# Kernel tuning notes

Measured on AMD Instinct MI355X. Metric: run time of the kernel, lower is better.

The kernel has to match this reference:

```python
import jax, jax.numpy as jnp
import numpy as np
import math

HEADS = 8
CH = 16  # hidden_channels per head
SCALE = 1.0 / math.sqrt(CH)


def _transformer_conv(x, src, dst, qw, qb, kw, kb, vw, vb, sw, sb):
    """PyG TransformerConv (concat=True, root_weight=True, eval mode -> no dropout)."""
    N = x.shape[0]
    q = (x @ qw + qb).reshape(N, HEADS, CH)
    k = (x @ kw + kb).reshape(N, HEADS, CH)
    v = (x @ vw + vb).reshape(N, HEADS, CH)
    # per-edge attention logits: message from src j to dst i
    alpha = jnp.sum(q[dst] * k[src], axis=-1) * SCALE        # [E, H]
    # segment softmax over incoming edges of each dst node
    m = jax.ops.segment_max(alpha, dst, num_segments=N)      # [N, H]
    a = jnp.exp(alpha - m[dst])                              # [E, H]
    denom = jax.ops.segment_sum(a, dst, num_segments=N)      # [N, H]
    a = a / denom[dst]
    msg = v[src] * a[:, :, None]                             # [E, H, C]
    out = jax.ops.segment_sum(msg, dst, num_segments=N).reshape(N, HEADS * CH)
    return out + x @ sw + sb  # skip connection (lin_skip)


def setup_inputs() -> dict:
    key = jax.random.key(0)
    ks = jax.random.split(key, 16)
    N, E, IN = 50000, 800000, 128
    D = HEADS * CH  # 128

    def lin(k, fi, fo):
        return (jax.random.normal(k, (fi, fo), jnp.float32) / math.sqrt(fi))

    inp = {
        "x": jax.random.normal(ks[0], (N, IN), jnp.float32),
        "edge_index": jax.random.randint(ks[1], (2, E), 0, N, dtype=jnp.int64),
        "edge_attr": jax.random.normal(ks[2], (E, 1), jnp.float32),
        # conv1: in_channels -> hidden*heads
        "q_w0": lin(ks[3], IN, D), "q_b0": jnp.zeros((D,), jnp.float32),
        "k_w0": lin(ks[4], IN, D), "k_b0": jnp.zeros((D,), jnp.float32),
        "v_w0": lin(ks[5], IN, D), "v_b0": jnp.zeros((D,), jnp.float32),
        "s_w0": lin(ks[6], IN, D), "s_b0": jnp.zeros((D,), jnp.float32),
        # conv2[0]: hidden*heads -> hidden*heads
        "q_w1": lin(ks[7], D, D), "q_b1": jnp.zeros((D,), jnp.float32),
        "k_w1": lin(ks[8], D, D), "k_b1": jnp.zeros((D,), jnp.float32),
        "v_w1": lin(ks[9], D, D), "v_b1": jnp.zeros((D,), jnp.float32),
        "s_w1": lin(ks[10], D, D), "s_b1": jnp.zeros((D,), jnp.float32),
    }
    return inp


def reference(x, edge_index, edge_attr,
              q_w0, q_b0, k_w0, k_b0, v_w0, v_b0, s_w0, s_b0,
              q_w1, q_b1, k_w1, k_b1, v_w1, v_b1, s_w1, s_b1):
    src, dst = edge_index[0], edge_index[1]
    # edge_attr is accepted but unused by the original forward
    h = _transformer_conv(x, src, dst, q_w0, q_b0, k_w0, k_b0, v_w0, v_b0, s_w0, s_b0)
    h = jax.nn.relu(h)
    h = _transformer_conv(h, src, dst, q_w1, q_b1, k_w1, k_b1, v_w1, v_b1, s_w1, s_b1)
    return h
```

## Files before the change

### kernel.cpp

```cpp
#include <hip/hip_runtime.h>
#include <math.h>


#define HEADS 8
#define CH 16
#define DM 128
#define SCALE 0.25f

typedef __attribute__((ext_vector_type(8))) short short8;
typedef __attribute__((ext_vector_type(4))) float floatx4;
typedef __attribute__((ext_vector_type(2))) float floatx2;

static __device__ __forceinline__ ushort f2bf(float f) {
    unsigned u = __float_as_uint(f);
    unsigned r = u + 0x7FFFu + ((u >> 16) & 1u);
    return (ushort)(r >> 16);
}
static __device__ __forceinline__ float bflo(unsigned u) {
    return __uint_as_float(u << 16);
}
static __device__ __forceinline__ float bfhi(unsigned u) {
    return __uint_as_float(u & 0xFFFF0000u);
}
static __device__ __forceinline__ unsigned pack2bf(float lo, float hi) {
    return (unsigned)f2bf(lo) | ((unsigned)f2bf(hi) << 16);
}
static __device__ __forceinline__ floatx2 fp8lo(unsigned v) {
    return __builtin_amdgcn_cvt_pk_f32_fp8(v, false);
}
static __device__ __forceinline__ floatx2 fp8hi(unsigned v) {
    return __builtin_amdgcn_cvt_pk_f32_fp8(v, true);
}

#define AP 136

static __device__ __forceinline__ void gemm_body(
    int bx, const float* __restrict__ Xf, const ushort* __restrict__ Xb,
    const ushort* __restrict__ WT,
    const float* __restrict__ bq, const float* __restrict__ bk,
    const float* __restrict__ bv, const float* __restrict__ bsk,
    ushort* __restrict__ Qb, ushort* __restrict__ Kb,
    unsigned char* __restrict__ Vq, ushort* __restrict__ Sb, int N,
    ushort* As)
{
    const int row0 = bx * 32;
    const int tid  = threadIdx.x;

    if (Xf) {
        #pragma unroll
        for (int i = 0; i < 2; ++i) {
            int id = tid + i * 512;
            int r = id >> 5, ch = id & 31;
            float4 v = make_float4(0.f, 0.f, 0.f, 0.f);
            if (row0 + r < N)
                v = *(const float4*)(Xf + (size_t)(row0 + r) * DM + ch * 4);
            ushort4 sv;
            sv.x = f2bf(v.x); sv.y = f2bf(v.y);
            sv.z = f2bf(v.z); sv.w = f2bf(v.w);
            *(ushort4*)(As + r * AP + ch * 4) = sv;
        }
    } else {
        int id = tid;
        int r = id >> 4, ch = id & 15;
        uint4 v = make_uint4(0, 0, 0, 0);
        if (row0 + r < N)
            v = *(const uint4*)(Xb + (size_t)(row0 + r) * DM + ch * 8);
        *(uint4*)(As + r * AP + ch * 8) = v;
    }
    __syncthreads();

    const int lane = tid & 63, w = tid >> 6;
    const int band = w & 3;
    const int m0   = (w >> 2) * 2;
    const int lr = lane & 15, lq = lane >> 4;

    short8 a[4][2];
    #pragma unroll
    for (int ks = 0; ks < 4; ++ks) {
        const int koff = ks * 32 + lq * 8;
        #pragma unroll
        for (int mt = 0; mt < 2; ++mt)
            a[ks][mt] = *(const short8*)(As + (mt * 16 + lr) * AP + koff);
    }

    #pragma unroll
    for (int mi = 0; mi < 2; ++mi) {
        const int mat = m0 + mi;
        const ushort* Wband = WT + (size_t)mat * 16384 + (size_t)band * 4096;
        const float* bias = (mat == 0) ? bq : (mat == 1) ? bk
                          : (mat == 2) ? bv : bsk;
        floatx4 acc[2][2] = {};
        #pragma unroll
        for (int ks = 0; ks < 4; ++ks) {
            short8 b[2];
            #pragma unroll
            for (int t = 0; t < 2; ++t)
                b[t] = *(const short8*)(Wband + (ks * 2 + t) * 512 + lane * 8);
            #pragma unroll
            for (int mt = 0; mt < 2; ++mt)
                #pragma unroll
                for (int nt = 0; nt < 2; ++nt)
                    acc[mt][nt] = __builtin_amdgcn_mfma_f32_16x16x32_bf16(
                        a[ks][mt], b[nt], acc[mt][nt], 0, 0, 0);
        }
        const int nq = band * 32;
        if (mat == 2) {
            #pragma unroll
            for (int nt = 0; nt < 2; ++nt) {
                const int col = nq + nt * 16 + lr;
                const float bcol = bias[col];
                #pragma unroll
                for (int mt = 0; mt < 2; ++mt) {
                    const int rbase = row0 + mt * 16 + lq * 4;
                    #pragma unroll
                    for (int r = 0; r < 4; ++r) {
                        const int row = rbase + r;
                        if (row < N) {
                            float v = acc[mt][nt][r] + bcol;
                            unsigned p = __builtin_amdgcn_cvt_pk_fp8_f32(
                                v, v, 0u, false);
                            Vq[(size_t)row * DM + col] = (unsigned char)p;
                        }
                    }
                }
            }
        } else {
            ushort* OutB = (mat == 0) ? Qb : (mat == 1) ? Kb : Sb;
            #pragma unroll
            for (int nt = 0; nt < 2; ++nt) {
                const int col = nq + nt * 16 + lr;
                const float bcol = bias[col];
                #pragma unroll
                for (int mt = 0; mt < 2; ++mt) {
                    const int rbase = row0 + mt * 16 + lq * 4;
                    #pragma unroll
                    for (int r = 0; r < 4; ++r) {
                        const int row = rbase + r;
                        if (row < N)
                            OutB[(size_t)row * DM + col] = f2bf(acc[mt][nt][r] + bcol);
                    }
                }
            }
        }
    }
}

__global__ __launch_bounds__(256)
void cvt_hist(const float* __restrict__ W0, const float* __restrict__ W1,
              const float* __restrict__ W2, const float* __restrict__ W3,
              const float* __restrict__ W4, const float* __restrict__ W5,
              const float* __restrict__ W6, const float* __restrict__ W7,
              ushort* __restrict__ WT,
              const int* __restrict__ dst, int* __restrict__ counts, int E)
{
    const int b = blockIdx.x;
    if (b < 512) {
        const float* Ws[8] = {W0, W1, W2, W3, W4, W5, W6, W7};
        const float* W = Ws[b >> 6];
        int idx = (b & 63) * 256 + threadIdx.x;
        int c    = idx >> 9;
        int s    = idx & 511;
        int lane = s >> 3, j = s & 7;
        int w  = c >> 3, ks = (c >> 1) & 3, t = c & 1;
        int n = w * 32 + t * 16 + (lane & 15);
        int k = ks * 32 + (lane >> 4) * 8 + j;
        WT[(size_t)(b >> 6) * 16384 + idx] = f2bf(W[k * 128 + n]);
    } else {
        int e4 = ((b - 512) * 256 + threadIdx.x) * 4;
        if (e4 + 3 < E) {
            const int4 d = *(const int4*)(dst + e4);
            atomicAdd(&counts[d.x], 1);
            atomicAdd(&counts[d.y], 1);
            atomicAdd(&counts[d.z], 1);
            atomicAdd(&counts[d.w], 1);
        } else {
            for (int e = e4; e < E; ++e) atomicAdd(&counts[dst[e]], 1);
        }
    }
}

__global__ __launch_bounds__(256)
void scan_p1(const int* __restrict__ counts, int* __restrict__ rowptr,
             int* __restrict__ bsums, int* __restrict__ dbins, int N)
{
    __shared__ int s[256];
    __shared__ int lb[256];
    const int t = threadIdx.x;
    const int base = blockIdx.x * 1024 + t * 4;
    lb[t] = 0;
    int c[4];
    int sum = 0;
    #pragma unroll
    for (int j = 0; j < 4; ++j) {
        c[j] = (base + j < N) ? counts[base + j] : 0;
        sum += c[j];
    }
    s[t] = sum;
    __syncthreads();
    #pragma unroll
    for (int j = 0; j < 4; ++j)
        if (base + j < N) atomicAdd(&lb[min(c[j], 255)], 1);
    for (int off = 1; off < 256; off <<= 1) {
        int v = (t >= off) ? s[t - off] : 0;
        __syncthreads();
        if (t >= off) s[t] += v;
        __syncthreads();
    }
    int ex = (t == 0) ? 0 : s[t - 1];
    #pragma unroll
    for (int j = 0; j < 4; ++j) {
        if (base + j < N) rowptr[base + j] = ex;
        ex += c[j];
    }
    if (t == 255) bsums[blockIdx.x] = s[255];
    if (lb[t] > 0) atomicAdd(&dbins[t], lb[t]);
}

__global__ __launch_bounds__(256)
void scan_p2(const int* __restrict__ bsums, int* __restrict__ bbase, int nb,
             const int* __restrict__ dbins, int* __restrict__ dcur)
{
    __shared__ int s[256];
    const int t = threadIdx.x;
    s[t] = (t < nb) ? bsums[t] : 0;
    __syncthreads();
    for (int off = 1; off < 256; off <<= 1) {
        int v = (t >= off) ? s[t - off] : 0;
        __syncthreads();
        if (t >= off) s[t] += v;
        __syncthreads();
    }
    if (t <= nb) bbase[t] = (t == 0) ? 0 : s[t - 1];
    __syncthreads();
    s[t] = dbins[255 - t];
    __syncthreads();
    for (int off = 1; off < 256; off <<= 1) {
        int v = (t >= off) ? s[t - off] : 0;
        __syncthreads();
        if (t >= off) s[t] += v;
        __syncthreads();
    }
    dcur[255 - t] = (t == 0) ? 0 : s[t - 1];
}

__global__ __launch_bounds__(256)
void scan_p3(int* __restrict__ rowptr, int* __restrict__ cursor,
             const int* __restrict__ bbase, int N, int nb)
{
    int i = blockIdx.x * 256 + threadIdx.x;
    if (i < N) {
        int v = rowptr[i] + bbase[i >> 10];
        rowptr[i] = v;
        cursor[i] = v;
    }
    if (i == 0) rowptr[N] = bbase[nb];
}

__global__ __launch_bounds__(512)
void gemm_scat(const float* __restrict__ Xf, const ushort* __restrict__ Xb,
               const ushort* __restrict__ WT,
               const float* __restrict__ bq, const float* __restrict__ bk,
               const float* __restrict__ bv, const float* __restrict__ bsk,
               ushort* __restrict__ Qb, ushort* __restrict__ Kb,
               unsigned char* __restrict__ Vq, ushort* __restrict__ Sb, int N,
               const int* __restrict__ src, const int* __restrict__ dst,
               int* __restrict__ cursor, int* __restrict__ esrc,
               const int* __restrict__ counts, int* __restrict__ dcur,
               int* __restrict__ perm, int E, int sb, int db)
{
    __shared__ ushort As[32 * AP];
    __shared__ int lc[256];
    __shared__ int lbase[256];

    const int b = blockIdx.x;
    if (b < sb) {
        int e4 = (b * 512 + (int)threadIdx.x) * 4;
        if (e4 + 3 < E) {
            const int4 s = *(const int4*)(src + e4);
            const int4 d = *(const int4*)(dst + e4);
            esrc[atomicAdd(&cursor[d.x], 1)] = s.x;
            esrc[atomicAdd(&cursor[d.y], 1)] = s.y;
            esrc[atomicAdd(&cursor[d.z], 1)] = s.z;
            esrc[atomicAdd(&cursor[d.w], 1)] = s.w;
        } else {
            for (int e = e4; e < E; ++e) {
                int pos = atomicAdd(&cursor[dst[e]], 1);
                esrc[pos] = src[e];
            }
        }
    } else if (b < sb + db) {
        const int t = threadIdx.x;
        if (t < 256) lc[t] = 0;
        __syncthreads();
        const int n = (b - sb) * 512 + t;
        int bin = 0, rank = 0;
        const bool valid = (n < N);
        if (valid) {
            bin = min(counts[n], 255);
            rank = atomicAdd(&lc[bin], 1);
        }
        __syncthreads();
        if (t < 256 && lc[t] > 0) lbase[t] = atomicAdd(&dcur[t], lc[t]);
        __syncthreads();
        if (valid) perm[lbase[bin] + rank] = n;
    } else {
        gemm_body(b - sb - db, Xf, Xb, WT, bq, bk, bv, bsk,
                  Qb, Kb, Vq, Sb, N, As);
    }
}

__global__ __launch_bounds__(512)
void gemm_mfma(const float* __restrict__ Xf, const ushort* __restrict__ Xb,
               const ushort* __restrict__ WT,
               const float* __restrict__ bq, const float* __restrict__ bk,
               const float* __restrict__ bv, const float* __restrict__ bsk,
               ushort* __restrict__ Qb, ushort* __restrict__ Kb,
               unsigned char* __restrict__ Vq, ushort* __restrict__ Sb, int N)
{
    __shared__ ushort As[32 * AP];
    gemm_body(blockIdx.x, Xf, Xb, WT, bq, bk, bv, bsk, Qb, Kb, Vq, Sb, N, As);
}

__global__ __launch_bounds__(256)
void node_attn(const ushort* __restrict__ Qb, const ushort* __restrict__ Kb,
               const unsigned char* __restrict__ Vq,
               const int* __restrict__ rowptr, const int* __restrict__ esrc,
               const int* __restrict__ perm,
               const ushort* __restrict__ Yb, float* __restrict__ Yout,
               ushort* __restrict__ Bout, int N, int relu)
{
    const int idx = blockIdx.x * 8 + (threadIdx.x >> 5);
    if (idx >= N) return;
    const int nid = perm[idx];
    const int c4 = (threadIdx.x & 31) * 4;
    const uint2 qv = *(const uint2*)(Qb + (size_t)nid * DM + c4);
    const float qx = bflo(qv.x), qy = bfhi(qv.x);
    const float qz = bflo(qv.y), qw = bfhi(qv.y);
    const int beg = rowptr[nid], end = rowptr[nid + 1];

    float lA = 0.f, lB = 0.f;
    float a0 = 0.f, a1 = 0.f, a2 = 0.f, a3 = 0.f;
    float b0 = 0.f, b1 = 0.f, b2 = 0.f, b3 = 0.f;

    int i = beg;
    for (; i + 7 < end; i += 8) {
        const int s0 = __builtin_nontemporal_load(esrc + i);
        const int s1 = __builtin_nontemporal_load(esrc + i + 1);
        const int s2 = __builtin_nontemporal_load(esrc + i + 2);
        const int s3 = __builtin_nontemporal_load(esrc + i + 3);
        const int s4 = __builtin_nontemporal_load(esrc + i + 4);
        const int s5 = __builtin_nontemporal_load(esrc + i + 5);
        const int s6 = __builtin_nontemporal_load(esrc + i + 6);
        const int s7 = __builtin_nontemporal_load(esrc + i + 7);
        const uint2 kA = *(const uint2*)(Kb + (size_t)s0 * DM + c4);
        const uint2 kB = *(const uint2*)(Kb + (size_t)s1 * DM + c4);
        const uint2 kC = *(const uint2*)(Kb + (size_t)s2 * DM + c4);
        const uint2 kD = *(const uint2*)(Kb + (size_t)s3 * DM + c4);
        const uint2 kE = *(const uint2*)(Kb + (size_t)s4 * DM + c4);
        const uint2 kF = *(const uint2*)(Kb + (size_t)s5 * DM + c4);
        const uint2 kG = *(const uint2*)(Kb + (size_t)s6 * DM + c4);
        const uint2 kH = *(const uint2*)(Kb + (size_t)s7 * DM + c4);
        const unsigned vA = *(const unsigned*)(Vq + (size_t)s0 * DM + c4);
        const unsigned vB = *(const unsigned*)(Vq + (size_t)s1 * DM + c4);
        const unsigned vC = *(const unsigned*)(Vq + (size_t)s2 * DM + c4);
        const unsigned vD = *(const unsigned*)(Vq + (size_t)s3 * DM + c4);
        const unsigned vE = *(const unsigned*)(Vq + (size_t)s4 * DM + c4);
        const unsigned vF = *(const unsigned*)(Vq + (size_t)s5 * DM + c4);
        const unsigned vG = *(const unsigned*)(Vq + (size_t)s6 * DM + c4);
        const unsigned vH = *(const unsigned*)(Vq + (size_t)s7 * DM + c4);
        float pA = qx * bflo(kA.x);
        pA = fmaf(qy, bfhi(kA.x), pA);
        pA = fmaf(qz, bflo(kA.y), pA);
        pA = fmaf(qw, bfhi(kA.y), pA);
        float pB = qx * bflo(kB.x);
        pB = fmaf(qy, bfhi(kB.x), pB);
        pB = fmaf(qz, bflo(kB.y), pB);
        pB = fmaf(qw, bfhi(kB.y), pB);
        float pC = qx * bflo(kC.x);
        pC = fmaf(qy, bfhi(kC.x), pC);
        pC = fmaf(qz, bflo(kC.y), pC);
        pC = fmaf(qw, bfhi(kC.y), pC);
        float pD = qx * bflo(kD.x);
        pD = fmaf(qy, bfhi(kD.x), pD);
        pD = fmaf(qz, bflo(kD.y), pD);
        pD = fmaf(qw, bfhi(kD.y), pD);
        float pE = qx * bflo(kE.x);
        pE = fmaf(qy, bfhi(kE.x), pE);
        pE = fmaf(qz, bflo(kE.y), pE);
        pE = fmaf(qw, bfhi(kE.y), pE);
        float pF = qx * bflo(kF.x);
        pF = fmaf(qy, bfhi(kF.x), pF);
        pF = fmaf(qz, bflo(kF.y), pF);
        pF = fmaf(qw, bfhi(kF.y), pF);
        float pG = qx * bflo(kG.x);
        pG = fmaf(qy, bfhi(kG.x), pG);
        pG = fmaf(qz, bflo(kG.y), pG);
        pG = fmaf(qw, bfhi(kG.y), pG);
        float pH = qx * bflo(kH.x);
        pH = fmaf(qy, bfhi(kH.x), pH);
        pH = fmaf(qz, bflo(kH.y), pH);
        pH = fmaf(qw, bfhi(kH.y), pH);
        pA += __shfl_xor(pA, 1, 4); pA += __shfl_xor(pA, 2, 4);
        pB += __shfl_xor(pB, 1, 4); pB += __shfl_xor(pB, 2, 4);
        pC += __shfl_xor(pC, 1, 4); pC += __shfl_xor(pC, 2, 4);
        pD += __shfl_xor(pD, 1, 4); pD += __shfl_xor(pD, 2, 4);
        pE += __shfl_xor(pE, 1, 4); pE += __shfl_xor(pE, 2, 4);
        pF += __shfl_xor(pF, 1, 4); pF += __shfl_xor(pF, 2, 4);
        pG += __shfl_xor(pG, 1, 4); pG += __shfl_xor(pG, 2, 4);
        pH += __shfl_xor(pH, 1, 4); pH += __shfl_xor(pH, 2, 4);
        const float wA = __expf(pA * SCALE);
        const float wB = __expf(pB * SCALE);
        const float wC = __expf(pC * SCALE);
        const float wD = __expf(pD * SCALE);
        const float wE = __expf(pE * SCALE);
        const float wF = __expf(pF * SCALE);
        const float wG = __expf(pG * SCALE);
        const float wH = __expf(pH * SCALE);
        lA += (wA + wC) + (wE + wG);
        lB += (wB + wD) + (wF + wH);
        {
            const floatx2 dA0 = fp8lo(vA), dA1 = fp8hi(vA);
            const floatx2 dB0 = fp8lo(vB), dB1 = fp8hi(vB);
            a0 = fmaf(wA, dA0.x, a0); b0 = fmaf(wB, dB0.x, b0);
            a1 = fmaf(wA, dA0.y, a1); b1 = fmaf(wB, dB0.y, b1);
            a2 = fmaf(wA, dA1.x, a2); b2 = fmaf(wB, dB1.x, b2);
            a3 = fmaf(wA, dA1.y, a3); b3 = fmaf(wB, dB1.y, b3);
        }
        {
            const floatx2 dC0 = fp8lo(vC), dC1 = fp8hi(vC);
            const floatx2 dD0 = fp8lo(vD), dD1 = fp8hi(vD);
            a0 = fmaf(wC, dC0.x, a0); b0 = fmaf(wD, dD0.x, b0);
            a1 = fmaf(wC, dC0.y, a1); b1 = fmaf(wD, dD0.y, b1);
            a2 = fmaf(wC, dC1.x, a2); b2 = fmaf(wD, dD1.x, b2);
            a3 = fmaf(wC, dC1.y, a3); b3 = fmaf(wD, dD1.y, b3);
        }
        {
            const floatx2 dE0 = fp8lo(vE), dE1 = fp8hi(vE);
            const floatx2 dF0 = fp8lo(vF), dF1 = fp8hi(vF);
            a0 = fmaf(wE, dE0.x, a0); b0 = fmaf(wF, dF0.x, b0);
            a1 = fmaf(wE, dE0.y, a1); b1 = fmaf(wF, dF0.y, b1);
            a2 = fmaf(wE, dE1.x, a2); b2 = fmaf(wF, dF1.x, b2);
            a3 = fmaf(wE, dE1.y, a3); b3 = fmaf(wF, dF1.y, b3);
        }
        {
            const floatx2 dG0 = fp8lo(vG), dG1 = fp8hi(vG);
            const floatx2 dH0 = fp8lo(vH), dH1 = fp8hi(vH);
            a0 = fmaf(wG, dG0.x, a0); b0 = fmaf(wH, dH0.x, b0);
            a1 = fmaf(wG, dG0.y, a1); b1 = fmaf(wH, dH0.y, b1);
            a2 = fmaf(wG, dG1.x, a2); b2 = fmaf(wH, dH1.x, b2);
            a3 = fmaf(wG, dG1.y, a3); b3 = fmaf(wH, dH1.y, b3);
        }
    }
    for (; i + 3 < end; i += 4) {
        const int s0 = __builtin_nontemporal_load(esrc + i);
        const int s1 = __builtin_nontemporal_load(esrc + i + 1);
        const int s2 = __builtin_nontemporal_load(esrc + i + 2);
        const int s3 = __builtin_nontemporal_load(esrc + i + 3);
        const uint2 kA = *(const uint2*)(Kb + (size_t)s0 * DM + c4);
        const uint2 kB = *(const uint2*)(Kb + (size_t)s1 * DM + c4);
        const uint2 kC = *(const uint2*)(Kb + (size_t)s2 * DM + c4);
        const uint2 kD = *(const uint2*)(Kb + (size_t)s3 * DM + c4);
        const unsigned vA = *(const unsigned*)(Vq + (size_t)s0 * DM + c4);
        const unsigned vB = *(const unsigned*)(Vq + (size_t)s1 * DM + c4);
        const unsigned vC = *(const unsigned*)(Vq + (size_t)s2 * DM + c4);
        const unsigned vD = *(const unsigned*)(Vq + (size_t)s3 * DM + c4);
        float pA = qx * bflo(kA.x);
        pA = fmaf(qy, bfhi(kA.x), pA);
        pA = fmaf(qz, bflo(kA.y), pA);
        pA = fmaf(qw, bfhi(kA.y), pA);
        float pB = qx * bflo(kB.x);
        pB = fmaf(qy, bfhi(kB.x), pB);
        pB = fmaf(qz, bflo(kB.y), pB);
        pB = fmaf(qw, bfhi(kB.y), pB);
        float pC = qx * bflo(kC.x);
        pC = fmaf(qy, bfhi(kC.x), pC);
        pC = fmaf(qz, bflo(kC.y), pC);
        pC = fmaf(qw, bfhi(kC.y), pC);
        float pD = qx * bflo(kD.x);
        pD = fmaf(qy, bfhi(kD.x), pD);
        pD = fmaf(qz, bflo(kD.y), pD);
        pD = fmaf(qw, bfhi(kD.y), pD);
        pA += __shfl_xor(pA, 1, 4); pA += __shfl_xor(pA, 2, 4);
        pB += __shfl_xor(pB, 1, 4); pB += __shfl_xor(pB, 2, 4);
        pC += __shfl_xor(pC, 1, 4); pC += __shfl_xor(pC, 2, 4);
        pD += __shfl_xor(pD, 1, 4); pD += __shfl_xor(pD, 2, 4);
        const float wA = __expf(pA * SCALE);
        const float wB = __expf(pB * SCALE);
        const float wC = __expf(pC * SCALE);
        const float wD = __expf(pD * SCALE);
        lA += wA + wC;
        lB += wB + wD;
        {
            const floatx2 dA0 = fp8lo(vA), dA1 = fp8hi(vA);
            const floatx2 dB0 = fp8lo(vB), dB1 = fp8hi(vB);
            a0 = fmaf(wA, dA0.x, a0); b0 = fmaf(wB, dB0.x, b0);
            a1 = fmaf(wA, dA0.y, a1); b1 = fmaf(wB, dB0.y, b1);
            a2 = fmaf(wA, dA1.x, a2); b2 = fmaf(wB, dB1.x, b2);
            a3 = fmaf(wA, dA1.y, a3); b3 = fmaf(wB, dB1.y, b3);
        }
        {
            const floatx2 dC0 = fp8lo(vC), dC1 = fp8hi(vC);
            const floatx2 dD0 = fp8lo(vD), dD1 = fp8hi(vD);
            a0 = fmaf(wC, dC0.x, a0); b0 = fmaf(wD, dD0.x, b0);
            a1 = fmaf(wC, dC0.y, a1); b1 = fmaf(wD, dD0.y, b1);
            a2 = fmaf(wC, dC1.x, a2); b2 = fmaf(wD, dD1.x, b2);
            a3 = fmaf(wC, dC1.y, a3); b3 = fmaf(wD, dD1.y, b3);
        }
    }
    for (; i < end; ++i) {
        const int s0 = __builtin_nontemporal_load(esrc + i);
        const uint2 kA = *(const uint2*)(Kb + (size_t)s0 * DM + c4);
        const unsigned vA = *(const unsigned*)(Vq + (size_t)s0 * DM + c4);
        float p = qx * bflo(kA.x);
        p = fmaf(qy, bfhi(kA.x), p);
        p = fmaf(qz, bflo(kA.y), p);
        p = fmaf(qw, bfhi(kA.y), p);
        p += __shfl_xor(p, 1, 4);
        p += __shfl_xor(p, 2, 4);
        const float wg = __expf(p * SCALE);
        lA += wg;
        const floatx2 dA0 = fp8lo(vA), dA1 = fp8hi(vA);
        a0 = fmaf(wg, dA0.x, a0);
        a1 = fmaf(wg, dA0.y, a1);
        a2 = fmaf(wg, dA1.x, a2);
        a3 = fmaf(wg, dA1.y, a3);
    }
    const float l = lA + lB;
    a0 += b0; a1 += b1; a2 += b2; a3 += b3;

    const float inv = (l > 0.f) ? 1.f / l : 0.f;
    const uint2 yb = *(const uint2*)(Yb + (size_t)nid * DM + c4);
    float y0 = fmaf(a0, inv, bflo(yb.x));
    float y1 = fmaf(a1, inv, bfhi(yb.x));
    float y2 = fmaf(a2, inv, bflo(yb.y));
    float y3 = fmaf(a3, inv, bfhi(yb.y));
    if (relu) {
        y0 = fmaxf(y0, 0.f); y1 = fmaxf(y1, 0.f);
        y2 = fmaxf(y2, 0.f); y3 = fmaxf(y3, 0.f);
    }
    if (Yout) {
        float4 o = make_float4(y0, y1, y2, y3);
        *(float4*)(Yout + (size_t)nid * DM + c4) = o;
    }
    if (Bout) {
        uint2 o;
        o.x = pack2bf(y0, y1);
        o.y = pack2bf(y2, y3);
        *(uint2*)(Bout + (size_t)nid * DM + c4) = o;
    }
}

extern "C" void kernel_launch(void* const* d_in, const int* in_sizes, int n_in,
                              void* d_out, int out_size, void* d_ws, size_t ws_size,
                              hipStream_t stream)
{
    const float* x   = (const float*)d_in[0];
    const int* eidx  = (const int*)d_in[1];
    const float* qw0 = (const float*)d_in[3];  const float* qb0 = (const float*)d_in[4];
    const float* kw0 = (const float*)d_in[5];  const float* kb0 = (const float*)d_in[6];
    const float* vw0 = (const float*)d_in[7];  const float* vb0 = (const float*)d_in[8];
    const float* sw0 = (const float*)d_in[9];  const float* sb0 = (const float*)d_in[10];
    const float* qw1 = (const float*)d_in[11]; const float* qb1 = (const float*)d_in[12];
    const float* kw1 = (const float*)d_in[13]; const float* kb1 = (const float*)d_in[14];
    const float* vw1 = (const float*)d_in[15]; const float* vb1 = (const float*)d_in[16];
    const float* sw1 = (const float*)d_in[17]; const float* sb1 = (const float*)d_in[18];

    const int N = in_sizes[0] / DM;
    const int E = in_sizes[1] / 2;
    const int* src = eidx;
    const int* dst = eidx + E;

    size_t nd  = (size_t)N * DM;
    ushort* Qb = (ushort*)d_ws;
    ushort* Kb = Qb + nd;
    ushort* Xb = Kb + nd;
    ushort* Sb = Xb + nd;
    ushort* WT = Sb + nd;
    unsigned char* Vq = (unsigned char*)(WT + 8 * 16384);
    int* counts = (int*)(Vq + nd);
    int* rowptr = counts + N;
    int* cursor = rowptr + (N + 1);
    int* esrc   = cursor + N;
    int* perm   = esrc + E;
    int* dbins  = perm + N;
    int* dcur   = dbins + 256;
    int* bsums  = dcur + 256;
    int* bbase  = bsums + 256;
    float* out  = (float*)d_out;

    const int nb = (N + 1023) / 1024;
    const int ggrid = (N + 31) / 32;
    const int ablk = (N + 7) / 8;
    const int sb = (E + 2047) / 2048;
    const int db = (N + 511) / 512;

    hipMemsetAsync(counts, 0, (size_t)N * sizeof(int), stream);
    hipMemsetAsync(dbins, 0, 256 * sizeof(int), stream);

    cvt_hist<<<512 + (E + 1023) / 1024, 256, 0, stream>>>(
        qw0, kw0, vw0, sw0, qw1, kw1, vw1, sw1, WT, dst, counts, E);

    scan_p1<<<nb, 256, 0, stream>>>(counts, rowptr, bsums, dbins, N);
    scan_p2<<<1, 256, 0, stream>>>(bsums, bbase, nb, dbins, dcur);
    scan_p3<<<(N + 255) / 256, 256, 0, stream>>>(rowptr, cursor, bbase, N, nb);

    gemm_scat<<<sb + db + ggrid, 512, 0, stream>>>(
        x, nullptr, WT, qb0, kb0, vb0, sb0, Qb, Kb, Vq, Sb, N,
        src, dst, cursor, esrc, counts, dcur, perm, E, sb, db);

    node_attn<<<ablk, 256, 0, stream>>>(Qb, Kb, Vq, rowptr, esrc, perm,
                                        Sb, nullptr, Xb, N, 1);

    gemm_mfma<<<ggrid, 512, 0, stream>>>(nullptr, Xb, WT + 4 * 16384,
                                         qb1, kb1, vb1, sb1,
                                         Qb, Kb, Vq, Sb, N);
    node_attn<<<ablk, 256, 0, stream>>>(Qb, Kb, Vq, rowptr, esrc, perm,
                                        Sb, out, nullptr, N, 0);
}
```

Measured before the change: 344.8 us.

## Pipeline layer-1 attention with layer-2 GEMM in chunks over permuted nodes

Splits the degree-sorted node ordering into three chunks and fuses attention for one chunk with the layer-2 projection GEMM of the previous chunk in a single launch. The GEMM now gathers input rows and scatters outputs through the perm array, and writes to separate second-layer Q/K/V/S buffers so the two layers do not alias. This aims to overlap the memory-bound attention with the MFMA GEMM and cut tail idle time. In exchange it adds extra workspace, indirect row addressing, and more launches.

```diff
diff --git a/kernel.cpp b/kernel.cpp
--- a/kernel.cpp
+++ b/kernel.cpp
@@ -41,7 +41,7 @@
     const float* __restrict__ bv, const float* __restrict__ bsk,
     ushort* __restrict__ Qb, ushort* __restrict__ Kb,
     unsigned char* __restrict__ Vq, ushort* __restrict__ Sb, int N,
-    ushort* As)
+    const int* __restrict__ prm, ushort* As)
 {
     const int row0 = bx * 32;
     const int tid  = threadIdx.x;
@@ -63,8 +63,10 @@
         int id = tid;
         int r = id >> 4, ch = id & 15;
         uint4 v = make_uint4(0, 0, 0, 0);
-        if (row0 + r < N)
-            v = *(const uint4*)(Xb + (size_t)(row0 + r) * DM + ch * 8);
+        if (row0 + r < N) {
+            int pr = prm ? prm[row0 + r] : (row0 + r);
+            v = *(const uint4*)(Xb + (size_t)pr * DM + ch * 8);
+        }
         *(uint4*)(As + r * AP + ch * 8) = v;
     }
     __syncthreads();
@@ -116,10 +118,11 @@
                     for (int r = 0; r < 4; ++r) {
                         const int row = rbase + r;
                         if (row < N) {
+                            const int pr = prm ? prm[row] : row;
                             float v = acc[mt][nt][r] + bcol;
                             unsigned p = __builtin_amdgcn_cvt_pk_fp8_f32(
                                 v, v, 0u, false);
-                            Vq[(size_t)row * DM + col] = (unsigned char)p;
+                            Vq[(size_t)pr * DM + col] = (unsigned char)p;
                         }
                     }
                 }
@@ -136,8 +139,10 @@
                     #pragma unroll
                     for (int r = 0; r < 4; ++r) {
                         const int row = rbase + r;
-                        if (row < N)
-                            OutB[(size_t)row * DM + col] = f2bf(acc[mt][nt][r] + bcol);
+                        if (row < N) {
+                            const int pr = prm ? prm[row] : row;
+                            OutB[(size_t)pr * DM + col] = f2bf(acc[mt][nt][r] + bcol);
+                        }
                     }
                 }
             }
@@ -145,192 +150,14 @@
     }
 }
 
-__global__ __launch_bounds__(256)
-void cvt_hist(const float* __restrict__ W0, const float* __restrict__ W1,
-              const float* __restrict__ W2, const float* __restrict__ W3,
-              const float* __restrict__ W4, const float* __restrict__ W5,
-              const float* __restrict__ W6, const float* __restrict__ W7,
-              ushort* __restrict__ WT,
-              const int* __restrict__ dst, int* __restrict__ counts, int E)
-{
-    const int b = blockIdx.x;
-    if (b < 512) {
-        const float* Ws[8] = {W0, W1, W2, W3, W4, W5, W6, W7};
-        const float* W = Ws[b >> 6];
-        int idx = (b & 63) * 256 + threadIdx.x;
-        int c    = idx >> 9;
-        int s    = idx & 511;
-        int lane = s >> 3, j = s & 7;
-        int w  = c >> 3, ks = (c >> 1) & 3, t = c & 1;
-        int n = w * 32 + t * 16 + (lane & 15);
-        int k = ks * 32 + (lane >> 4) * 8 + j;
-        WT[(size_t)(b >> 6) * 16384 + idx] = f2bf(W[k * 128 + n]);
-    } else {
-        int e4 = ((b - 512) * 256 + threadIdx.x) * 4;
-        if (e4 + 3 < E) {
-            const int4 d = *(const int4*)(dst + e4);
-            atomicAdd(&counts[d.x], 1);
-            atomicAdd(&counts[d.y], 1);
-            atomicAdd(&counts[d.z], 1);
-            atomicAdd(&counts[d.w], 1);
-        } else {
-            for (int e = e4; e < E; ++e) atomicAdd(&counts[dst[e]], 1);
-        }
-    }
-}
-
-__global__ __launch_bounds__(256)
-void scan_p1(const int* __restrict__ counts, int* __restrict__ rowptr,
-             int* __restrict__ bsums, int* __restrict__ dbins, int N)
-{
-    __shared__ int s[256];
-    __shared__ int lb[256];
-    const int t = threadIdx.x;
-    const int base = blockIdx.x * 1024 + t * 4;
-    lb[t] = 0;
-    int c[4];
-    int sum = 0;
-    #pragma unroll
-    for (int j = 0; j < 4; ++j) {
-        c[j] = (base + j < N) ? counts[base + j] : 0;
-        sum += c[j];
-    }
-    s[t] = sum;
-    __syncthreads();
-    #pragma unroll
-    for (int j = 0; j < 4; ++j)
-        if (base + j < N) atomicAdd(&lb[min(c[j], 255)], 1);
-    for (int off = 1; off < 256; off <<= 1) {
-        int v = (t >= off) ? s[t - off] : 0;
-        __syncthreads();
-        if (t >= off) s[t] += v;
-        __syncthreads();
-    }
-    int ex = (t == 0) ? 0 : s[t - 1];
-    #pragma unroll
-    for (int j = 0; j < 4; ++j) {
-        if (base + j < N) rowptr[base + j] = ex;
-        ex += c[j];
-    }
-    if (t == 255) bsums[blockIdx.x] = s[255];
-    if (lb[t] > 0) atomicAdd(&dbins[t], lb[t]);
-}
-
-__global__ __launch_bounds__(256)
-void scan_p2(const int* __restrict__ bsums, int* __restrict__ bbase, int nb,
-             const int* __restrict__ dbins, int* __restrict__ dcur)
-{
-    __shared__ int s[256];
-    const int t = threadIdx.x;
-    s[t] = (t < nb) ? bsums[t] : 0;
-    __syncthreads();
-    for (int off = 1; off < 256; off <<= 1) {
-        int v = (t >= off) ? s[t - off] : 0;
-        __syncthreads();
-        if (t >= off) s[t] += v;
-        __syncthreads();
-    }
-    if (t <= nb) bbase[t] = (t == 0) ? 0 : s[t - 1];
-    __syncthreads();
-    s[t] = dbins[255 - t];
-    __syncthreads();
-    for (int off = 1; off < 256; off <<= 1) {
-        int v = (t >= off) ? s[t - off] : 0;
-        __syncthreads();
-        if (t >= off) s[t] += v;
-        __syncthreads();
-    }
-    dcur[255 - t] = (t == 0) ? 0 : s[t - 1];
-}
-
-__global__ __launch_bounds__(256)
-void scan_p3(int* __restrict__ rowptr, int* __restrict__ cursor,
-             const int* __restrict__ bbase, int N, int nb)
-{
-    int i = blockIdx.x * 256 + threadIdx.x;
-    if (i < N) {
-        int v = rowptr[i] + bbase[i >> 10];
-        rowptr[i] = v;
-        cursor[i] = v;
-    }
-    if (i == 0) rowptr[N] = bbase[nb];
-}
-
-__global__ __launch_bounds__(512)
-void gemm_scat(const float* __restrict__ Xf, const ushort* __restrict__ Xb,
-               const ushort* __restrict__ WT,
-               const float* __restrict__ bq, const float* __restrict__ bk,
-               const float* __restrict__ bv, const float* __restrict__ bsk,
-               ushort* __restrict__ Qb, ushort* __restrict__ Kb,
-               unsigned char* __restrict__ Vq, ushort* __restrict__ Sb, int N,
-               const int* __restrict__ src, const int* __restrict__ dst,
-               int* __restrict__ cursor, int* __restrict__ esrc,
-               const int* __restrict__ counts, int* __restrict__ dcur,
-               int* __restrict__ perm, int E, int sb, int db)
-{
-    __shared__ ushort As[32 * AP];
-    __shared__ int lc[256];
-    __shared__ int lbase[256];
-
-    const int b = blockIdx.x;
-    if (b < sb) {
-        int e4 = (b * 512 + (int)threadIdx.x) * 4;
-        if (e4 + 3 < E) {
-            const int4 s = *(const int4*)(src + e4);
-            const int4 d = *(const int4*)(dst + e4);
-            esrc[atomicAdd(&cursor[d.x], 1)] = s.x;
-            esrc[atomicAdd(&cursor[d.y], 1)] = s.y;
-            esrc[atomicAdd(&cursor[d.z], 1)] = s.z;
-            esrc[atomicAdd(&cursor[d.w], 1)] = s.w;
-        } else {
-            for (int e = e4; e < E; ++e) {
-                int pos = atomicAdd(&cursor[dst[e]], 1);
-                esrc[pos] = src[e];
-            }
-        }
-    } else if (b < sb + db) {
-        const int t = threadIdx.x;
-        if (t < 256) lc[t] = 0;
-        __syncthreads();
-        const int n = (b - sb) * 512 + t;
-        int bin = 0, rank = 0;
-        const bool valid = (n < N);
-        if (valid) {
-            bin = min(counts[n], 255);
-            rank = atomicAdd(&lc[bin], 1);
-        }
-        __syncthreads();
-        if (t < 256 && lc[t] > 0) lbase[t] = atomicAdd(&dcur[t], lc[t]);
-        __syncthreads();
-        if (valid) perm[lbase[bin] + rank] = n;
-    } else {
-        gemm_body(b - sb - db, Xf, Xb, WT, bq, bk, bv, bsk,
-                  Qb, Kb, Vq, Sb, N, As);
-    }
-}
-
-__global__ __launch_bounds__(512)
-void gemm_mfma(const float* __restrict__ Xf, const ushort* __restrict__ Xb,
-               const ushort* __restrict__ WT,
-               const float* __restrict__ bq, const float* __restrict__ bk,
-               const float* __restrict__ bv, const float* __restrict__ bsk,
-               ushort* __restrict__ Qb, ushort* __restrict__ Kb,
-               unsigned char* __restrict__ Vq, ushort* __restrict__ Sb, int N)
-{
-    __shared__ ushort As[32 * AP];
-    gemm_body(blockIdx.x, Xf, Xb, WT, bq, bk, bv, bsk, Qb, Kb, Vq, Sb, N, As);
-}
-
-__global__ __launch_bounds__(256)
-void node_attn(const ushort* __restrict__ Qb, const ushort* __restrict__ Kb,
-               const unsigned char* __restrict__ Vq,
-               const int* __restrict__ rowptr, const int* __restrict__ esrc,
-               const int* __restrict__ perm,
-               const ushort* __restrict__ Yb, float* __restrict__ Yout,
-               ushort* __restrict__ Bout, int N, int relu)
-{
-    const int idx = blockIdx.x * 8 + (threadIdx.x >> 5);
-    if (idx >= N) return;
+static __device__ __forceinline__ void attn_node(
+    int idx, const ushort* __restrict__ Qb, const ushort* __restrict__ Kb,
+    const unsigned char* __restrict__ Vq,
+    const int* __restrict__ rowptr, const int* __restrict__ esrc,
+    const int* __restrict__ perm,
+    const ushort* __restrict__ Yb, float* __restrict__ Yout,
+    ushort* __restrict__ Bout, int N, int relu)
+{
     const int nid = perm[idx];
     const int c4 = (threadIdx.x & 31) * 4;
     const uint2 qv = *(const uint2*)(Qb + (size_t)nid * DM + c4);
@@ -550,6 +377,225 @@
     }
 }
 
+__global__ __launch_bounds__(256)
+void cvt_hist(const float* __restrict__ W0, const float* __restrict__ W1,
+              const float* __restrict__ W2, const float* __restrict__ W3,
+              const float* __restrict__ W4, const float* __restrict__ W5,
+              const float* __restrict__ W6, const float* __restrict__ W7,
+              ushort* __restrict__ WT,
+              const int* __restrict__ dst, int* __restrict__ counts, int E)
+{
+    const int b = blockIdx.x;
+    if (b < 512) {
+        const float* Ws[8] = {W0, W1, W2, W3, W4, W5, W6, W7};
+        const float* W = Ws[b >> 6];
+        int idx = (b & 63) * 256 + threadIdx.x;
+        int c    = idx >> 9;
+        int s    = idx & 511;
+        int lane = s >> 3, j = s & 7;
+        int w  = c >> 3, ks = (c >> 1) & 3, t = c & 1;
+        int n = w * 32 + t * 16 + (lane & 15);
+        int k = ks * 32 + (lane >> 4) * 8 + j;
+        WT[(size_t)(b >> 6) * 16384 + idx] = f2bf(W[k * 128 + n]);
+    } else {
+        int e4 = ((b - 512) * 256 + threadIdx.x) * 4;
+        if (e4 + 3 < E) {
+            const int4 d = *(const int4*)(dst + e4);
+            atomicAdd(&counts[d.x], 1);
+            atomicAdd(&counts[d.y], 1);
+            atomicAdd(&counts[d.z], 1);
+            atomicAdd(&counts[d.w], 1);
+        } else {
+            for (int e = e4; e < E; ++e) atomicAdd(&counts[dst[e]], 1);
+        }
+    }
+}
+
+__global__ __launch_bounds__(256)
+void scan_p1(const int* __restrict__ counts, int* __restrict__ rowptr,
+             int* __restrict__ bsums, int* __restrict__ dbins, int N)
+{
+    __shared__ int s[256];
+    __shared__ int lb[256];
+    const int t = threadIdx.x;
+    const int base = blockIdx.x * 1024 + t * 4;
+    lb[t] = 0;
+    int c[4];
+    int sum = 0;
+    #pragma unroll
+    for (int j = 0; j < 4; ++j) {
+        c[j] = (base + j < N) ? counts[base + j] : 0;
+        sum += c[j];
+    }
+    s[t] = sum;
+    __syncthreads();
+    #pragma unroll
+    for (int j = 0; j < 4; ++j)
+        if (base + j < N) atomicAdd(&lb[min(c[j], 255)], 1);
+    for (int off = 1; off < 256; off <<= 1) {
+        int v = (t >= off) ? s[t - off] : 0;
+        __syncthreads();
+        if (t >= off) s[t] += v;
+        __syncthreads();
+    }
+    int ex = (t == 0) ? 0 : s[t - 1];
+    #pragma unroll
+    for (int j = 0; j < 4; ++j) {
+        if (base + j < N) rowptr[base + j] = ex;
+        ex += c[j];
+    }
+    if (t == 255) bsums[blockIdx.x] = s[255];
+    if (lb[t] > 0) atomicAdd(&dbins[t], lb[t]);
+}
+
+__global__ __launch_bounds__(256)
+void scan_p2(const int* __restrict__ bsums, int* __restrict__ bbase, int nb,
+             const int* __restrict__ dbins, int* __restrict__ dcur)
+{
+    __shared__ int s[256];
+    const int t = threadIdx.x;
+    s[t] = (t < nb) ? bsums[t] : 0;
+    __syncthreads();
+    for (int off = 1; off < 256; off <<= 1) {
+        int v = (t >= off) ? s[t - off] : 0;
+        __syncthreads();
+        if (t >= off) s[t] += v;
+        __syncthreads();
+    }
+    if (t <= nb) bbase[t] = (t == 0) ? 0 : s[t - 1];
+    __syncthreads();
+    s[t] = dbins[255 - t];
+    __syncthreads();
+    for (int off = 1; off < 256; off <<= 1) {
+        int v = (t >= off) ? s[t - off] : 0;
+        __syncthreads();
+        if (t >= off) s[t] += v;
+        __syncthreads();
+    }
+    dcur[255 - t] = (t == 0) ? 0 : s[t - 1];
+}
+
+__global__ __launch_bounds__(256)
+void scan_p3(int* __restrict__ rowptr, int* __restrict__ cursor,
+             const int* __restrict__ bbase, int N, int nb)
+{
+    int i = blockIdx.x * 256 + threadIdx.x;
+    if (i < N) {
+        int v = rowptr[i] + bbase[i >> 10];
+        rowptr[i] = v;
+        cursor[i] = v;
+    }
+    if (i == 0) rowptr[N] = bbase[nb];
+}
+
+__global__ __launch_bounds__(512)
+void gemm_scat(const float* __restrict__ Xf, const ushort* __restrict__ Xb,
+               const ushort* __restrict__ WT,
+               const float* __restrict__ bq, const float* __restrict__ bk,
+               const float* __restrict__ bv, const float* __restrict__ bsk,
+               ushort* __restrict__ Qb, ushort* __restrict__ Kb,
+               unsigned char* __restrict__ Vq, ushort* __restrict__ Sb, int N,
+               const int* __restrict__ src, const int* __restrict__ dst,
+               int* __restrict__ cursor, int* __restrict__ esrc,
+               const int* __restrict__ counts, int* __restrict__ dcur,
+               int* __restrict__ perm, int E, int sb, int db)
+{
+    __shared__ ushort As[32 * AP];
+    __shared__ int lc[256];
+    __shared__ int lbase[256];
+
+    const int b = blockIdx.x;
+    if (b < sb) {
+        int e4 = (b * 512 + (int)threadIdx.x) * 4;
+        if (e4 + 3 < E) {
+            const int4 s = *(const int4*)(src + e4);
+            const int4 d = *(const int4*)(dst + e4);
+            esrc[atomicAdd(&cursor[d.x], 1)] = s.x;
+            esrc[atomicAdd(&cursor[d.y], 1)] = s.y;
+            esrc[atomicAdd(&cursor[d.z], 1)] = s.z;
+            esrc[atomicAdd(&cursor[d.w], 1)] = s.w;
+        } else {
+            for (int e = e4; e < E; ++e) {
+                int pos = atomicAdd(&cursor[dst[e]], 1);
+                esrc[pos] = src[e];
+            }
+        }
+    } else if (b < sb + db) {
+        const int t = threadIdx.x;
+        if (t < 256) lc[t] = 0;
+        __syncthreads();
+        const int n = (b - sb) * 512 + t;
+        int bin = 0, rank = 0;
+        const bool valid = (n < N);
+        if (valid) {
+            bin = min(counts[n], 255);
+            rank = atomicAdd(&lc[bin], 1);
+        }
+        __syncthreads();
+        if (t < 256 && lc[t] > 0) lbase[t] = atomicAdd(&dcur[t], lc[t]);
+        __syncthreads();
+        if (valid) perm[lbase[bin] + rank] = n;
+    } else {
+        gemm_body(b - sb - db, Xf, Xb, WT, bq, bk, bv, bsk,
+                  Qb, Kb, Vq, Sb, N, nullptr, As);
+    }
+}
+
+__global__ __launch_bounds__(512)
+void gemm_mfma(const float* __restrict__ Xf, const ushort* __restrict__ Xb,
+               const ushort* __restrict__ WT,
+               const float* __restrict__ bq, const float* __restrict__ bk,
+               const float* __restrict__ bv, const float* __restrict__ bsk,
+               ushort* __restrict__ Qb, ushort* __restrict__ Kb,
+               unsigned char* __restrict__ Vq, ushort* __restrict__ Sb, int N,
+               const int* __restrict__ prm, int tile0)
+{
+    __shared__ ushort As[32 * AP];
+    gemm_body(tile0 + blockIdx.x, Xf, Xb, WT, bq, bk, bv, bsk,
+              Qb, Kb, Vq, Sb, N, prm, As);
+}
+
+__global__ __launch_bounds__(256)
+void node_attn(const ushort* __restrict__ Qb, const ushort* __restrict__ Kb,
+               const unsigned char* __restrict__ Vq,
+               const int* __restrict__ rowptr, const int* __restrict__ esrc,
+               const int* __restrict__ perm,
+               const ushort* __restrict__ Yb, float* __restrict__ Yout,
+               ushort* __restrict__ Bout, int N, int relu,
+               int idx0, int idx1)
+{
+    const int idx = idx0 + blockIdx.x * 8 + (threadIdx.x >> 5);
+    if (idx >= idx1) return;
+    attn_node(idx, Qb, Kb, Vq, rowptr, esrc, perm, Yb, Yout, Bout, N, relu);
+}
+
+__global__ __launch_bounds__(512)
+void attn_gemm(const ushort* __restrict__ Qb1, const ushort* __restrict__ Kb1,
+               const unsigned char* __restrict__ Vq1,
+               const int* __restrict__ rowptr, const int* __restrict__ esrc,
+               const int* __restrict__ perm,
+               const ushort* __restrict__ Sb1, ushort* __restrict__ Xb,
+               int N, int relu, int aIdx0, int aIdx1, int aB,
+               const ushort* __restrict__ WT2,
+               const float* __restrict__ bq, const float* __restrict__ bk,
+               const float* __restrict__ bv, const float* __restrict__ bsk,
+               ushort* __restrict__ Qb2, ushort* __restrict__ Kb2,
+               unsigned char* __restrict__ Vq2, ushort* __restrict__ Sb2,
+               int tile0)
+{
+    __shared__ ushort As[32 * AP];
+    const int b = blockIdx.x;
+    if (b < aB) {
+        const int idx = aIdx0 + b * 16 + (threadIdx.x >> 5);
+        if (idx < aIdx1)
+            attn_node(idx, Qb1, Kb1, Vq1, rowptr, esrc, perm,
+                      Sb1, nullptr, Xb, N, relu);
+    } else {
+        gemm_body(tile0 + (b - aB), nullptr, Xb, WT2, bq, bk, bv, bsk,
+                  Qb2, Kb2, Vq2, Sb2, N, perm, As);
+    }
+}
+
 extern "C" void kernel_launch(void* const* d_in, const int* in_sizes, int n_in,
                               void* d_out, int out_size, void* d_ws, size_t ws_size,
                               hipStream_t stream)
@@ -588,9 +634,17 @@
     int* bbase  = bsums + 256;
     float* out  = (float*)d_out;
 
+    uintptr_t p2 = ((uintptr_t)(bbase + 257) + 255) & ~(uintptr_t)255;
+    ushort* Qb2 = (ushort*)p2;
+    ushort* Kb2 = Qb2 + nd;
+    ushort* Sb2 = Kb2 + nd;
+    unsigned char* Vq2 = (unsigned char*)(Sb2 + nd);
+    uintptr_t pend = (uintptr_t)(Vq2 + nd);
+    const bool pipelined =
+        (pend <= (uintptr_t)d_ws + ws_size) && (N >= 96);
+
     const int nb = (N + 1023) / 1024;
     const int ggrid = (N + 31) / 32;
-    const int ablk = (N + 7) / 8;
     const int sb = (E + 2047) / 2048;
     const int db = (N + 511) / 512;
 
@@ -608,12 +662,41 @@
         x, nullptr, WT, qb0, kb0, vb0, sb0, Qb, Kb, Vq, Sb, N,
         src, dst, cursor, esrc, counts, dcur, perm, E, sb, db);
 
-    node_attn<<<ablk, 256, 0, stream>>>(Qb, Kb, Vq, rowptr, esrc, perm,
-                                        Sb, nullptr, Xb, N, 1);
-
-    gemm_mfma<<<ggrid, 512, 0, stream>>>(nullptr, Xb, WT + 4 * 16384,
-                                         qb1, kb1, vb1, sb1,
-                                         Qb, Kb, Vq, Sb, N);
-    node_attn<<<ablk, 256, 0, stream>>>(Qb, Kb, Vq, rowptr, esrc, perm,
-                                        Sb, out, nullptr, N, 0);
-}
+    if (pipelined) {
+        const int CHNK = ((N + 2) / 3 + 31) & ~31;
+        const int s1 = CHNK, s2 = 2 * CHNK;
+        const int e1 = (s2 < N) ? s2 : N;
+        const int len1 = e1 - s1, len2 = N - s2;
+        const int g0 = CHNK / 32;
+        const int g1 = (len1 + 31) / 32;
+        const int g2 = (len2 + 31) / 32;
+
+        node_attn<<<(CHNK + 7) / 8, 256, 0, stream>>>(
+            Qb, Kb, Vq, rowptr, esrc, perm, Sb, nullptr, Xb, N, 1, 0, CHNK);
+        {
+            const int aB = (len1 + 15) / 16;
+            attn_gemm<<<aB + g0, 512, 0, stream>>>(
+                Qb, Kb, Vq, rowptr, esrc, perm, Sb, Xb, N, 1, s1, e1, aB,
+                WT + 4 * 16384, qb1, kb1, vb1, sb1, Qb2, Kb2, Vq2, Sb2, 0);
+        }
+        {
+            const int aB = (len2 + 15) / 16;
+            attn_gemm<<<aB + g1, 512, 0, stream>>>(
+                Qb, Kb, Vq, rowptr, esrc, perm, Sb, Xb, N, 1, s2, N, aB,
+                WT + 4 * 16384, qb1, kb1, vb1, sb1, Qb2, Kb2, Vq2, Sb2, g0);
+        }
+        gemm_mfma<<<g2, 512, 0, stream>>>(
+            nullptr, Xb, WT + 4 * 16384, qb1, kb1, vb1, sb1,
+            Qb2, Kb2, Vq2, Sb2, N, perm, g0 + g1);
+        node_attn<<<(N + 7) / 8, 256, 0, stream>>>(
+            Qb2, Kb2, Vq2, rowptr, esrc, perm, Sb2, out, nullptr, N, 0, 0, N);
+    } else {
+        node_attn<<<(N + 7) / 8, 256, 0, stream>>>(
+            Qb, Kb, Vq, rowptr, esrc, perm, Sb, nullptr, Xb, N, 1, 0, N);
+        gemm_mfma<<<ggrid, 512, 0, stream>>>(
+            nullptr, Xb, WT + 4 * 16384, qb1, kb1, vb1, sb1,
+            Qb, Kb, Vq, Sb, N, nullptr, 0);
+        node_attn<<<(N + 7) / 8, 256, 0, stream>>>(
+            Qb, Kb, Vq, rowptr, esrc, perm, Sb, out, nullptr, N, 0, 0, N);
+    }
+}
```

New measurement: 375.3 us. 1.09x slower.

## Replace global-atomic edge scatter with two-level bucketed CSR build

Applied to the files above, without the earlier changes.

The per-edge global atomic scatter into the CSR is replaced by a two-pass scheme. First, edges are grouped into 256-node buckets using block-local shared-memory counters plus one global atomic per bucket per block. A new escat2 kernel then places each edge within its bucket using shared-memory atomics. This is meant to cut contended scattered global atomics and random writes, at the cost of an extra kernel launch, an extra pass over an E-sized buffer, and packing that assumes N ≤ 65536.

```diff
diff --git a/kernel.cpp b/kernel.cpp
--- a/kernel.cpp
+++ b/kernel.cpp
@@ -111,10 +111,10 @@
                 const float bcol = bias[col];
                 #pragma unroll
                 for (int mt = 0; mt < 2; ++mt) {
-                    const int rbase = row0 + mt * 16 + lq * 4;
+                    const int rbase0 = row0 + mt * 16 + lq * 4;
                     #pragma unroll
                     for (int r = 0; r < 4; ++r) {
-                        const int row = rbase + r;
+                        const int row = rbase0 + r;
                         if (row < N) {
                             float v = acc[mt][nt][r] + bcol;
                             unsigned p = __builtin_amdgcn_cvt_pk_fp8_f32(
@@ -132,10 +132,10 @@
                 const float bcol = bias[col];
                 #pragma unroll
                 for (int mt = 0; mt < 2; ++mt) {
-                    const int rbase = row0 + mt * 16 + lq * 4;
+                    const int rbase0 = row0 + mt * 16 + lq * 4;
                     #pragma unroll
                     for (int r = 0; r < 4; ++r) {
-                        const int row = rbase + r;
+                        const int row = rbase0 + r;
                         if (row < N)
                             OutB[(size_t)row * DM + col] = f2bf(acc[mt][nt][r] + bcol);
                     }
@@ -245,13 +245,15 @@
 
 __global__ __launch_bounds__(256)
 void scan_p3(int* __restrict__ rowptr, int* __restrict__ cursor,
-             const int* __restrict__ bbase, int N, int nb)
+             const int* __restrict__ bbase, int* __restrict__ bcur,
+             int N, int nb)
 {
     int i = blockIdx.x * 256 + threadIdx.x;
     if (i < N) {
         int v = rowptr[i] + bbase[i >> 10];
         rowptr[i] = v;
         cursor[i] = v;
+        if ((i & 255) == 0) bcur[i >> 8] = v;
     }
     if (i == 0) rowptr[N] = bbase[nb];
 }
@@ -265,8 +267,9 @@
                unsigned char* __restrict__ Vq, ushort* __restrict__ Sb, int N,
                const int* __restrict__ src, const int* __restrict__ dst,
                int* __restrict__ cursor, int* __restrict__ esrc,
+               int* __restrict__ ebuf, int* __restrict__ bcur,
                const int* __restrict__ counts, int* __restrict__ dcur,
-               int* __restrict__ perm, int E, int sb, int db)
+               int* __restrict__ perm, int E, int sb, int db, int bucketed)
 {
     __shared__ ushort As[32 * AP];
     __shared__ int lc[256];
@@ -274,18 +277,53 @@
 
     const int b = blockIdx.x;
     if (b < sb) {
-        int e4 = (b * 512 + (int)threadIdx.x) * 4;
-        if (e4 + 3 < E) {
-            const int4 s = *(const int4*)(src + e4);
-            const int4 d = *(const int4*)(dst + e4);
-            esrc[atomicAdd(&cursor[d.x], 1)] = s.x;
-            esrc[atomicAdd(&cursor[d.y], 1)] = s.y;
-            esrc[atomicAdd(&cursor[d.z], 1)] = s.z;
-            esrc[atomicAdd(&cursor[d.w], 1)] = s.w;
+        if (bucketed) {
+            const int t = threadIdx.x;
+            if (t < 256) lc[t] = 0;
+            __syncthreads();
+            int e4 = (b * 512 + t) * 4;
+            int pk[4], bkt[4];
+            int ne = 0;
+            if (e4 + 3 < E) {
+                const int4 s = *(const int4*)(src + e4);
+                const int4 d = *(const int4*)(dst + e4);
+                pk[0] = (s.x & 0xFFFF) | ((d.x & 255) << 16); bkt[0] = d.x >> 8;
+                pk[1] = (s.y & 0xFFFF) | ((d.y & 255) << 16); bkt[1] = d.y >> 8;
+                pk[2] = (s.z & 0xFFFF) | ((d.z & 255) << 16); bkt[2] = d.z >> 8;
+                pk[3] = (s.w & 0xFFFF) | ((d.w & 255) << 16); bkt[3] = d.w >> 8;
+                ne = 4;
+            } else {
+                for (int e = e4; e < E; ++e) {
+                    int sv = src[e], dv = dst[e];
+                    pk[ne] = (sv & 0xFFFF) | ((dv & 255) << 16);
+                    bkt[ne] = dv >> 8;
+                    ++ne;
+                }
+            }
+            for (int j = 0; j < ne; ++j) atomicAdd(&lc[bkt[j]], 1);
+            __syncthreads();
+            if (t < 256 && lc[t] > 0) lbase[t] = atomicAdd(&bcur[t], lc[t]);
+            __syncthreads();
+            if (t < 256) lc[t] = 0;
+            __syncthreads();
+            for (int j = 0; j < ne; ++j) {
+                int r = atomicAdd(&lc[bkt[j]], 1);
+                ebuf[lbase[bkt[j]] + r] = pk[j];
+            }
         } else {
-            for (int e = e4; e < E; ++e) {
-                int pos = atomicAdd(&cursor[dst[e]], 1);
-                esrc[pos] = src[e];
+            int e4 = (b * 512 + (int)threadIdx.x) * 4;
+            if (e4 + 3 < E) {
+                const int4 s = *(const int4*)(src + e4);
+                const int4 d = *(const int4*)(dst + e4);
+                esrc[atomicAdd(&cursor[d.x], 1)] = s.x;
+                esrc[atomicAdd(&cursor[d.y], 1)] = s.y;
+                esrc[atomicAdd(&cursor[d.z], 1)] = s.z;
+                esrc[atomicAdd(&cursor[d.w], 1)] = s.w;
+            } else {
+                for (int e = e4; e < E; ++e) {
+                    int pos = atomicAdd(&cursor[dst[e]], 1);
+                    esrc[pos] = src[e];
+                }
             }
         }
     } else if (b < sb + db) {
@@ -306,6 +344,28 @@
     } else {
         gemm_body(b - sb - db, Xf, Xb, WT, bq, bk, bv, bsk,
                   Qb, Kb, Vq, Sb, N, As);
+    }
+}
+
+__global__ __launch_bounds__(256)
+void escat2(const int* __restrict__ rowptr, const int* __restrict__ ebuf,
+            int* __restrict__ esrc, int N)
+{
+    __shared__ int rbase[257];
+    __shared__ int cur[256];
+    const int b = blockIdx.x, t = threadIdx.x;
+    const int n0 = b * 256;
+    const int nn = min(256, N - n0);
+    rbase[t] = rowptr[min(n0 + t, N)];
+    cur[t] = 0;
+    if (t == 0) rbase[256] = rowptr[min(n0 + 256, N)];
+    __syncthreads();
+    const int r0 = rbase[0], r1 = rbase[nn];
+    for (int i = r0 + t; i < r1; i += 256) {
+        const int e = ebuf[i];
+        const int dr = e >> 16;
+        const int rank = atomicAdd(&cur[dr], 1);
+        esrc[rbase[dr] + rank] = e & 0xFFFF;
     }
 }
 
@@ -586,7 +646,14 @@
     int* dcur   = dbins + 256;
     int* bsums  = dcur + 256;
     int* bbase  = bsums + 256;
+    int* ebuf   = bbase + 257;
+    int* bcur   = ebuf + E;
     float* out  = (float*)d_out;
+
+    const int nbuck = (N + 255) >> 8;
+    const bool bucketed =
+        (N <= 65536) && (nbuck <= 256) &&
+        ((uintptr_t)(bcur + 256) <= (uintptr_t)d_ws + ws_size);
 
     const int nb = (N + 1023) / 1024;
     const int ggrid = (N + 31) / 32;
@@ -602,11 +669,16 @@
 
     scan_p1<<<nb, 256, 0, stream>>>(counts, rowptr, bsums, dbins, N);
     scan_p2<<<1, 256, 0, stream>>>(bsums, bbase, nb, dbins, dcur);
-    scan_p3<<<(N + 255) / 256, 256, 0, stream>>>(rowptr, cursor, bbase, N, nb);
+    scan_p3<<<(N + 255) / 256, 256, 0, stream>>>(rowptr, cursor, bbase, bcur,
+                                                 N, nb);
 
     gemm_scat<<<sb + db + ggrid, 512, 0, stream>>>(
         x, nullptr, WT, qb0, kb0, vb0, sb0, Qb, Kb, Vq, Sb, N,
-        src, dst, cursor, esrc, counts, dcur, perm, E, sb, db);
+        src, dst, cursor, esrc, ebuf, bcur, counts, dcur, perm,
+        E, sb, db, bucketed ? 1 : 0);
+
+    if (bucketed)
+        escat2<<<nbuck, 256, 0, stream>>>(rowptr, ebuf, esrc, N);
 
     node_attn<<<ablk, 256, 0, stream>>>(Qb, Kb, Vq, rowptr, esrc, perm,
                                         Sb, nullptr, Xb, N, 1);
```

New measurement: 335.2 us. 2.8% less time.
